# Kernel tuning notes

Hardware: AMD Instinct MI355X
Metric: run time of the kernel (lower is better)

## Reference

```python
import jax, jax.numpy as jnp
import numpy as np


def setup_inputs() -> dict:
    key = jax.random.key(0)
    k1, k2, k3 = jax.random.split(key, 3)
    B, N, D = 8, 4096, 64
    q = jax.random.normal(k1, (B, N, D), dtype=jnp.float32)
    k = jax.random.normal(k2, (B, N, D), dtype=jnp.float32)
    v = jax.random.normal(k3, (B, N, D), dtype=jnp.float32)
    attn_mask = jnp.ones((B, N), dtype=jnp.int32)  # 1 = attend, 0 = padding
    return {"q": q, "k": k, "v": v, "attn_mask": attn_mask}


def reference(q, k, v, attn_mask):
    # q: [B, n_q, d], k/v: [B, n_k, d], attn_mask: [B, n_k]
    d = q.shape[-1]
    n_q, n_k = q.shape[1], k.shape[1]
    scale = jnp.sqrt(jnp.asarray(d, dtype=q.dtype))
    # [B, n_q, n_k] attention logits
    logits = jnp.einsum("bqd,bkd->bqk", q, k) / scale
    # causal (mask_future=True): tril keep-mask over (n_q, n_k)
    causal = jnp.tril(jnp.ones((n_q, n_k), dtype=bool))
    neg_inf = jnp.asarray(-jnp.inf, dtype=logits.dtype)
    logits = jnp.where(causal[None, :, :], logits, neg_inf)
    # padding mask broadcast over query dim: [B, 1, n_k]
    logits = jnp.where(attn_mask[:, None, :] == 0, neg_inf, logits)
    w = jax.nn.softmax(logits, axis=-1)
    return jnp.einsum("bqk,bkd->bqd", w, v)
```

## Files before the change

### kernel.cpp

```cpp
#include <hip/hip_runtime.h>


#define BATCH 8
#define SEQ   4096
#define DIM   64
#define QT    64
#define NKT   (SEQ / 64)

typedef __attribute__((ext_vector_type(8))) short bf16x8;
typedef __attribute__((ext_vector_type(4))) float f32x4;

__device__ inline short f2bf(float f) {
    unsigned u = __builtin_bit_cast(unsigned, f);
    u += 0x7FFFu + ((u >> 16) & 1u);
    return (short)(u >> 16);
}

__device__ inline unsigned pk2bf(float a, float b) {
    unsigned ua = __builtin_bit_cast(unsigned, a) + 0x8000u;
    unsigned ub = __builtin_bit_cast(unsigned, b) + 0x8000u;
    return __builtin_amdgcn_perm(ub, ua, 0x07060302u);
}

__device__ inline float fast_exp2(float x) {
#if __has_builtin(__builtin_amdgcn_exp2f)
    return __builtin_amdgcn_exp2f(x);
#else
    return exp2f(x);
#endif
}

__device__ inline void gl_lds16(const void* g, void* l) {
    __builtin_amdgcn_global_load_lds(
        (const __attribute__((address_space(1))) void*)g,
        (__attribute__((address_space(3))) void*)l, 16, 0, 0);
}

__global__ __launch_bounds__(256)
void prep_kv(const float* __restrict__ kg, const float* __restrict__ vg,
             short* __restrict__ kw, short* __restrict__ vw) {
    const int tile = blockIdx.x;
    const float* kp = kg + (size_t)tile * 64 * DIM;
    const float* vp = vg + (size_t)tile * 64 * DIM;
    short* ko = kw + (size_t)tile * 4096;
    short* vo = vw + (size_t)tile * 4096;
    const int t = threadIdx.x;
#pragma unroll
    for (int i = 0; i < 4; ++i) {
        const int flat = i * 256 + t;
        const int key = flat >> 4, d0 = (flat & 15) * 4;
        const float4 kv = *(const float4*)(kp + (size_t)key * DIM + d0);
        uint2 kpk;
        kpk.x = pk2bf(kv.x, kv.y); kpk.y = pk2bf(kv.z, kv.w);
        *(uint2*)(ko + (((d0 >> 3) << 6) + key) * 8 + (d0 & 7)) = kpk;
        const float4 vv = *(const float4*)(vp + (size_t)key * DIM + d0);
        const int kc = key >> 3, jk = key & 7;
        vo[((kc << 6) + d0 + 0) * 8 + jk] = f2bf(vv.x);
        vo[((kc << 6) + d0 + 1) * 8 + jk] = f2bf(vv.y);
        vo[((kc << 6) + d0 + 2) * 8 + jk] = f2bf(vv.z);
        vo[((kc << 6) + d0 + 3) * 8 + jk] = f2bf(vv.w);
    }
}

template <bool WS>
__global__ __launch_bounds__(512, 4)
void attn_fwd(const float* __restrict__ qg, const float* __restrict__ kg,
              const float* __restrict__ vg, const int* __restrict__ mg,
              float* __restrict__ og, const short* __restrict__ kw,
              const short* __restrict__ vw) {
    __shared__ __align__(16) char smem[59392];
    short* KbS = (short*)smem;
    short* VbS = (short*)(smem + 16384);
    short* PbS = (short*)(smem + 32768);
    float* Ml  = (float*)(smem + 43008);
    float* OX = (float*)smem;
    float* LB = (float*)(smem + 16384);

    const int t    = threadIdx.x;
    const int w    = t >> 6;
    const int L    = t & 63;
    const int c15  = L & 15;
    const int quad = L >> 4;
    const int qsub = w & 3;
    const int kh   = w >> 2;

    const int id = blockIdx.x;
    const int b  = id & 7;
    const int j  = id >> 3;
    const int qb = (j < 32) ? (63 - j) : (j - 32);
    const int qbase  = qb * QT;
    const int ntiles = qb + 1;

    const float* qp = qg + (size_t)b * SEQ * DIM;
    const float* kp = kg + (size_t)b * SEQ * DIM;
    const float* vp = vg + (size_t)b * SEQ * DIM;
    const int*   mp = mg + (size_t)b * SEQ;
    const short* kwb = WS ? kw + (size_t)b * NKT * 4096 : nullptr;
    const short* vwb = WS ? vw + (size_t)b * NKT * 4096 : nullptr;

    const int qrow = qbase + qsub * 16 + c15;
    const float qscale = 0.125f * 1.44269504088896340736f;

    bf16x8 Qf[2];
#pragma unroll
    for (int c = 0; c < 2; ++c) {
        const float* src = qp + (size_t)qrow * DIM + c * 32 + quad * 8;
        float4 x = *(const float4*)(src);
        float4 y = *(const float4*)(src + 4);
        bf16x8 f;
        f[0] = f2bf(x.x * qscale); f[1] = f2bf(x.y * qscale);
        f[2] = f2bf(x.z * qscale); f[3] = f2bf(x.w * qscale);
        f[4] = f2bf(y.x * qscale); f[5] = f2bf(y.y * qscale);
        f[6] = f2bf(y.z * qscale); f[7] = f2bf(y.w * qscale);
        Qf[c] = f;
    }

    auto stage = [&](int bs, int kt) {
        const short* ks = kwb + (size_t)kt * 4096;
        const short* vs = vwb + (size_t)kt * 4096;
        const int off = w << 9;
        gl_lds16(ks + off + (L << 3), KbS + bs * 4096 + off);
        gl_lds16(vs + off + (L << 3), VbS + bs * 4096 + off);
    };

    for (int i = t; i < ntiles * 64; i += 512)
        Ml[i] = mp[i] ? 0.0f : -1e30f;

    float lsum = 0.0f;
    f32x4 Oacc[4];
#pragma unroll
    for (int nb = 0; nb < 4; ++nb) Oacc[nb] = (f32x4){0.f, 0.f, 0.f, 0.f};

    if constexpr (WS) stage(0, 0);

    short* Pw = PbS + w * 640;

    for (int kt = 0; kt < ntiles; ++kt) {
        const int cur = WS ? (kt & 1) : 0;

        if constexpr (!WS) {
            __syncthreads();
#pragma unroll
            for (int it = 0; it < 2; ++it) {
                const int flat = it * 512 + t;
                const int key = flat >> 4, d0 = (flat & 15) * 4;
                const float4 kv = *(const float4*)(kp + (size_t)(kt * 64 + key) * DIM + d0);
                uint2 kk;
                kk.x = pk2bf(kv.x, kv.y); kk.y = pk2bf(kv.z, kv.w);
                *(uint2*)&KbS[(((d0 >> 3) << 6) + key) * 8 + (d0 & 7)] = kk;
                const float4 vv = *(const float4*)(vp + (size_t)(kt * 64 + key) * DIM + d0);
                const int kc = key >> 3, jk = key & 7;
                VbS[((kc << 6) + d0 + 0) * 8 + jk] = f2bf(vv.x);
                VbS[((kc << 6) + d0 + 1) * 8 + jk] = f2bf(vv.y);
                VbS[((kc << 6) + d0 + 2) * 8 + jk] = f2bf(vv.z);
                VbS[((kc << 6) + d0 + 3) * 8 + jk] = f2bf(vv.w);
            }
            __syncthreads();
        } else {
            __syncthreads();
            if (kt + 1 < ntiles) stage(cur ^ 1, kt + 1);
        }

        const short* Kt = KbS + cur * 4096;
        const short* Vt = VbS + cur * 4096;

        f32x4 sacc[2];
        sacc[0] = (f32x4){0.f, 0.f, 0.f, 0.f};
        sacc[1] = (f32x4){0.f, 0.f, 0.f, 0.f};
#pragma unroll
        for (int c = 0; c < 2; ++c) {
#pragma unroll
            for (int i = 0; i < 2; ++i) {
                bf16x8 kf = *(const bf16x8*)&Kt[(((quad + 4 * c) << 6) + (2 * kh + i) * 16 + c15) * 8];
                sacc[i] = __builtin_amdgcn_mfma_f32_16x16x32_bf16(kf, Qf[c], sacc[i], 0, 0, 0);
            }
        }

        const bool diag = (kt == ntiles - 1);
#pragma unroll
        for (int i = 0; i < 2; ++i) {
            const int kb = 2 * kh + i;
            const float4 ma = *(const float4*)&Ml[kt * 64 + kb * 16 + quad * 4];
            const float mar[4] = {ma.x, ma.y, ma.z, ma.w};
            float p[4];
#pragma unroll
            for (int r = 0; r < 4; ++r) {
                float s = sacc[i][r] + mar[r];
                if (diag) {
                    const int keyg = kt * 64 + kb * 16 + quad * 4 + r;
                    if (keyg > qrow) s = -1e30f;
                }
                p[r] = fast_exp2(fminf(s, 80.0f));
                lsum += p[r];
            }
            uint2 pp;
            pp.x = pk2bf(p[0], p[1]);
            pp.y = pk2bf(p[2], p[3]);
            *(uint2*)&Pw[c15 * 40 + i * 16 + quad * 4] = pp;
        }

        bf16x8 pf = *(const bf16x8*)&Pw[c15 * 40 + quad * 8];
#pragma unroll
        for (int nb = 0; nb < 4; ++nb) {
            bf16x8 vf = *(const bf16x8*)&Vt[(((kh * 4 + quad) << 6) + nb * 16 + c15) * 8];
            Oacc[nb] = __builtin_amdgcn_mfma_f32_16x16x32_bf16(pf, vf, Oacc[nb], 0, 0, 0);
        }
    }

    lsum += __shfl_xor(lsum, 16);
    lsum += __shfl_xor(lsum, 32);

    __syncthreads();
    if (w >= 4) {
        const int g = w & 3;
#pragma unroll
        for (int r = 0; r < 4; ++r) {
            const int q = quad * 4 + r;
#pragma unroll
            for (int nb = 0; nb < 4; ++nb)
                OX[(g * 16 + q) * 64 + nb * 16 + c15] = Oacc[nb][r];
        }
        if (quad == 0) LB[g * 16 + c15] = lsum;
    }
    __syncthreads();
    if (w < 4) {
        const float inv = 1.0f / (lsum + LB[w * 16 + c15]);
        float* op = og + (size_t)b * SEQ * DIM;
#pragma unroll
        for (int r = 0; r < 4; ++r) {
            const float ir = __shfl(inv, (L & 48) + ((L & 48) >> 2) + r);
            const int row = qbase + w * 16 + quad * 4 + r;
#pragma unroll
            for (int nb = 0; nb < 4; ++nb)
                op[(size_t)row * DIM + nb * 16 + c15] =
                    (Oacc[nb][r] + OX[(w * 16 + quad * 4 + r) * 64 + nb * 16 + c15]) * ir;
        }
    }
}

extern "C" void kernel_launch(void* const* d_in, const int* in_sizes, int n_in,
                              void* d_out, int out_size, void* d_ws, size_t ws_size,
                              hipStream_t stream) {
    (void)in_sizes; (void)n_in; (void)out_size;
    const float* q = (const float*)d_in[0];
    const float* k = (const float*)d_in[1];
    const float* v = (const float*)d_in[2];
    const int*   m = (const int*)d_in[3];
    float* o = (float*)d_out;
    const size_t need = (size_t)BATCH * NKT * 4096 * sizeof(short) * 2;
    if (ws_size >= need) {
        short* kw = (short*)d_ws;
        short* vw = kw + (size_t)BATCH * NKT * 4096;
        prep_kv<<<dim3(BATCH * NKT), 256, 0, stream>>>(k, v, kw, vw);
        attn_fwd<true><<<dim3(512), 512, 0, stream>>>(q, k, v, m, o, kw, vw);
    } else {
        attn_fwd<false><<<dim3(512), 512, 0, stream>>>(q, k, v, m, o, nullptr, nullptr);
    }
}
```

Measured before the change: 131.8 us.

## Split long causal query tiles across blocks and merge partial results

```diff
diff --git a/kernel.cpp b/kernel.cpp
--- a/kernel.cpp
+++ b/kernel.cpp
@@ -62,6 +62,204 @@
     }
 }
 
+__global__ __launch_bounds__(512, 4)
+void attn_split(const float* __restrict__ qg, const int* __restrict__ mg,
+                float* __restrict__ og, const short* __restrict__ kw,
+                const short* __restrict__ vw, float* __restrict__ opart,
+                float* __restrict__ lpart) {
+    __shared__ __align__(16) char smem[59392];
+    short* KbS = (short*)smem;
+    short* VbS = (short*)(smem + 16384);
+    short* PbS = (short*)(smem + 32768);
+    float* Ml  = (float*)(smem + 43008);
+    float* OX = (float*)smem;
+    float* LB = (float*)(smem + 16384);
+
+    const int t    = threadIdx.x;
+    const int w    = t >> 6;
+    const int L    = t & 63;
+    const int c15  = L & 15;
+    const int quad = L >> 4;
+    const int qsub = w & 3;
+    const int kh   = w >> 2;
+
+    const int id   = blockIdx.x;
+    const int b    = id & 7;
+    const int r_   = id >> 3;
+    const int j    = r_ & 31;
+    const int sblk = r_ >> 5;
+    const int qL   = 63 - j;
+
+    const float* qp = qg + (size_t)b * SEQ * DIM;
+    const int*   mp = mg + (size_t)b * SEQ;
+    const short* kwb = kw + (size_t)b * NKT * 4096;
+    const short* vwb = vw + (size_t)b * NKT * 4096;
+    const float qscale = 0.125f * 1.44269504088896340736f;
+
+    auto stage = [&](int bs, int kt) {
+        const short* ks = kwb + (size_t)kt * 4096;
+        const short* vs = vwb + (size_t)kt * 4096;
+        const int off = w << 9;
+        gl_lds16(ks + off + (L << 3), KbS + bs * 4096 + off);
+        gl_lds16(vs + off + (L << 3), VbS + bs * 4096 + off);
+    };
+
+    short* Pw  = PbS + w * 640;
+    float* lqs = lpart + (size_t)(b * 32 + j) * 128;
+    float* osl = opart + (size_t)(b * 32 + j) * 4096;
+
+    const int nseg = (sblk == 0) ? 1 : 2;
+    for (int seg = 0; seg < nseg; ++seg) {
+        int qt, kt0, kt1, mode;
+        if (sblk == 0)     { qt = qL; kt0 = 0;  kt1 = 33;     mode = 0; }
+        else if (seg == 0) { qt = qL; kt0 = 33; kt1 = qL + 1; mode = 1; }
+        else               { qt = j;  kt0 = 0;  kt1 = j + 1;  mode = 2; }
+
+        const int qbase = qt * QT;
+        const int qrow  = qbase + qsub * 16 + c15;
+
+        bf16x8 Qf[2];
+#pragma unroll
+        for (int c = 0; c < 2; ++c) {
+            const float* src = qp + (size_t)qrow * DIM + c * 32 + quad * 8;
+            float4 x = *(const float4*)(src);
+            float4 y = *(const float4*)(src + 4);
+            bf16x8 f;
+            f[0] = f2bf(x.x * qscale); f[1] = f2bf(x.y * qscale);
+            f[2] = f2bf(x.z * qscale); f[3] = f2bf(x.w * qscale);
+            f[4] = f2bf(y.x * qscale); f[5] = f2bf(y.y * qscale);
+            f[6] = f2bf(y.z * qscale); f[7] = f2bf(y.w * qscale);
+            Qf[c] = f;
+        }
+
+        for (int i = t; i < (kt1 - kt0) * 64; i += 512) {
+            const int key = kt0 * 64 + i;
+            Ml[key] = mp[key] ? 0.0f : -1e30f;
+        }
+
+        float lsum = 0.0f;
+        f32x4 Oacc[4];
+#pragma unroll
+        for (int nb = 0; nb < 4; ++nb) Oacc[nb] = (f32x4){0.f, 0.f, 0.f, 0.f};
+
+        if (kt1 > kt0) stage(0, kt0);
+
+        for (int kt = kt0; kt < kt1; ++kt) {
+            const int cur = (kt - kt0) & 1;
+            __syncthreads();
+            if (kt + 1 < kt1) stage(cur ^ 1, kt + 1);
+
+            const short* Kt = KbS + cur * 4096;
+            const short* Vt = VbS + cur * 4096;
+
+            f32x4 sacc[2];
+            sacc[0] = (f32x4){0.f, 0.f, 0.f, 0.f};
+            sacc[1] = (f32x4){0.f, 0.f, 0.f, 0.f};
+#pragma unroll
+            for (int c = 0; c < 2; ++c) {
+#pragma unroll
+                for (int i = 0; i < 2; ++i) {
+                    bf16x8 kf = *(const bf16x8*)&Kt[(((quad + 4 * c) << 6) + (2 * kh + i) * 16 + c15) * 8];
+                    sacc[i] = __builtin_amdgcn_mfma_f32_16x16x32_bf16(kf, Qf[c], sacc[i], 0, 0, 0);
+                }
+            }
+
+            const bool diag = (kt == qt);
+#pragma unroll
+            for (int i = 0; i < 2; ++i) {
+                const int kb = 2 * kh + i;
+                const float4 ma = *(const float4*)&Ml[kt * 64 + kb * 16 + quad * 4];
+                const float mar[4] = {ma.x, ma.y, ma.z, ma.w};
+                float p[4];
+#pragma unroll
+                for (int r = 0; r < 4; ++r) {
+                    float s = sacc[i][r] + mar[r];
+                    if (diag) {
+                        const int keyg = kt * 64 + kb * 16 + quad * 4 + r;
+                        if (keyg > qrow) s = -1e30f;
+                    }
+                    p[r] = fast_exp2(fminf(s, 80.0f));
+                    lsum += p[r];
+                }
+                uint2 pp;
+                pp.x = pk2bf(p[0], p[1]);
+                pp.y = pk2bf(p[2], p[3]);
+                *(uint2*)&Pw[c15 * 40 + i * 16 + quad * 4] = pp;
+            }
+
+            bf16x8 pf = *(const bf16x8*)&Pw[c15 * 40 + quad * 8];
+#pragma unroll
+            for (int nb = 0; nb < 4; ++nb) {
+                bf16x8 vf = *(const bf16x8*)&Vt[(((kh * 4 + quad) << 6) + nb * 16 + c15) * 8];
+                Oacc[nb] = __builtin_amdgcn_mfma_f32_16x16x32_bf16(pf, vf, Oacc[nb], 0, 0, 0);
+            }
+        }
+
+        lsum += __shfl_xor(lsum, 16);
+        lsum += __shfl_xor(lsum, 32);
+
+        __syncthreads();
+        if (w >= 4) {
+            const int g = w & 3;
+#pragma unroll
+            for (int r = 0; r < 4; ++r) {
+                const int q = quad * 4 + r;
+#pragma unroll
+                for (int nb = 0; nb < 4; ++nb)
+                    OX[(g * 16 + q) * 64 + nb * 16 + c15] = Oacc[nb][r];
+            }
+            if (quad == 0) LB[g * 16 + c15] = lsum;
+        }
+        __syncthreads();
+        if (w < 4) {
+            const float ltot = lsum + LB[w * 16 + c15];
+            const float inv  = 1.0f / ltot;
+            float* dst = (mode == 1) ? osl
+                                     : og + ((size_t)b * SEQ + qbase) * DIM;
+            if (mode != 2 && L < 16)
+                lqs[(mode == 1 ? 64 : 0) + w * 16 + L] = ltot;
+#pragma unroll
+            for (int r = 0; r < 4; ++r) {
+                const float ir = (mode == 2)
+                    ? __shfl(inv, (L & 48) + ((L & 48) >> 2) + r) : 1.0f;
+                const int rl = w * 16 + quad * 4 + r;
+#pragma unroll
+                for (int nb = 0; nb < 4; ++nb)
+                    dst[(size_t)rl * DIM + nb * 16 + c15] =
+                        (Oacc[nb][r] + OX[rl * 64 + nb * 16 + c15]) * ir;
+            }
+        }
+        __syncthreads();
+    }
+}
+
+__global__ __launch_bounds__(256)
+void merge_ql(float* __restrict__ og, const float* __restrict__ opart,
+              const float* __restrict__ lpart) {
+    const int id = blockIdx.x;
+    const int b = id & 7, j = id >> 3;
+    const int qL = 63 - j;
+    const float* sp = opart + (size_t)(b * 32 + j) * 4096;
+    const float* lp = lpart + (size_t)(b * 32 + j) * 128;
+    float* op = og + ((size_t)b * SEQ + (size_t)qL * 64) * DIM;
+    const int t = threadIdx.x;
+#pragma unroll
+    for (int i = 0; i < 4; ++i) {
+        const int flat = i * 256 + t;
+        const int row = flat >> 4;
+        const int c4  = (flat & 15) * 4;
+        const float inv = 1.0f / (lp[row] + lp[64 + row]);
+        const float4 a = *(const float4*)(op + (size_t)row * DIM + c4);
+        const float4 p = *(const float4*)(sp + (size_t)row * 64 + c4);
+        float4 r;
+        r.x = (a.x + p.x) * inv;
+        r.y = (a.y + p.y) * inv;
+        r.z = (a.z + p.z) * inv;
+        r.w = (a.w + p.w) * inv;
+        *(float4*)(op + (size_t)row * DIM + c4) = r;
+    }
+}
+
 template <bool WS>
 __global__ __launch_bounds__(512, 4)
 void attn_fwd(const float* __restrict__ qg, const float* __restrict__ kg,
@@ -247,8 +445,21 @@
     const float* v = (const float*)d_in[2];
     const int*   m = (const int*)d_in[3];
     float* o = (float*)d_out;
-    const size_t need = (size_t)BATCH * NKT * 4096 * sizeof(short) * 2;
-    if (ws_size >= need) {
+
+    const size_t needKV    = (size_t)BATCH * NKT * 4096 * sizeof(short) * 2;
+    const size_t opartB    = (size_t)BATCH * 32 * 4096 * sizeof(float);
+    const size_t lpartB    = (size_t)BATCH * 32 * 128 * sizeof(float);
+    const size_t needSplit = needKV + opartB + lpartB;
+
+    if (ws_size >= needSplit) {
+        short* kw = (short*)d_ws;
+        short* vw = kw + (size_t)BATCH * NKT * 4096;
+        float* opart = (float*)((char*)d_ws + needKV);
+        float* lpart = opart + (size_t)BATCH * 32 * 4096;
+        prep_kv<<<dim3(BATCH * NKT), 256, 0, stream>>>(k, v, kw, vw);
+        attn_split<<<dim3(512), 512, 0, stream>>>(q, m, o, kw, vw, opart, lpart);
+        merge_ql<<<dim3(256), 256, 0, stream>>>(o, opart, lpart);
+    } else if (ws_size >= needKV) {
         short* kw = (short*)d_ws;
         short* vw = kw + (size_t)BATCH * NKT * 4096;
         prep_kv<<<dim3(BATCH * NKT), 256, 0, stream>>>(k, v, kw, vw);
```

Measured after the change: 124.7 us. -5.4%, faster.
